# Optimization experiments

Hardware: AMD Instinct MI355X
Metric: run time of the kernel (lower is better)

The kernel has to match this reference:

```python
import jax, jax.numpy as jnp
import numpy as np

B, H, L, N = 8, 512, 2048, 64  # batch, channels (vmapped width), seq len (l_max), state size
DT_MIN, DT_MAX = 0.01, 1.0


def setup_inputs() -> dict:
    key = jax.random.key(0)
    k1, k2, k3 = jax.random.split(key, 3)
    u = jax.random.normal(k1, (B, H, L), dtype=jnp.float32)
    # 'lin' scaling init: A_re = -0.5, A_im = pi * arange(N), per channel
    A_re = -0.5 * jnp.ones((H, N), jnp.float32)
    A_im = jnp.pi * jnp.broadcast_to(jnp.arange(N, dtype=jnp.float32), (H, N))
    C = jax.random.normal(k2, (H, N, 2), jnp.float32) * jnp.float32(0.5 ** 0.5)
    D = jnp.ones((H,), jnp.float32)
    log_step = (jax.random.uniform(k3, (H,), jnp.float32)
                * (jnp.log(DT_MAX) - jnp.log(DT_MIN)) + jnp.log(DT_MIN))
    return dict(u=u, A_re=A_re, A_im=A_im, C=C, D=D, log_step=log_step)


def reference(u, A_re, A_im, C, D, log_step):
    Lq = u.shape[-1]
    # A = clip(A_re, max=-1e-4) + i*A_im  (H, N) complex
    A = jnp.minimum(A_re, -1e-4) + 1j * A_im
    Cc = C[..., 0] + 1j * C[..., 1]                 # (H, N)
    step = jnp.exp(log_step)                        # (H,)
    dtA = step[:, None] * A                         # (H, N)
    # ZOH kernel: K[h,l] = Re( sum_n C[h,n] * (exp(dtA)-1)/A * exp(dtA)^l )
    coef = Cc * (jnp.exp(dtA) - 1.0) / A            # (H, N)
    ells = jnp.arange(Lq, dtype=jnp.float32)
    expmat = jnp.exp(dtA[:, :, None] * ells)        # (H, N, L) complex
    K = jnp.einsum('hn,hnl->hl', coef, expmat).real  # (H, L)
    # FFT causal convolution: pad to 2L (as in the original: pad u by len(K), K by len(u))
    n2 = 2 * Lq
    Ud = jnp.fft.rfft(u, n=n2, axis=-1)             # (B, H, L+1)
    Kd = jnp.fft.rfft(K, n=n2, axis=-1)             # (H, L+1)
    conv = jnp.fft.irfft(Ud * Kd[None], n=n2, axis=-1)[..., :Lq]
    return conv + D[None, :, None] * u
```

## Files before the change

### kernel.cpp

```cpp
#include <hip/hip_runtime.h>
#include <math.h>


typedef short bf16x8 __attribute__((ext_vector_type(8)));
typedef float f32x4  __attribute__((ext_vector_type(4)));

#define NCHK 32
#define USTR 68
#define ESTR 72

__device__ __forceinline__ short f2bf(float x){
    unsigned u = __float_as_uint(x);
    u += 0x7FFFu + ((u >> 16) & 1u);
    return (short)(u >> 16);
}
__device__ __forceinline__ float bf2f(short h){
    return __uint_as_float(((unsigned)(unsigned short)h) << 16);
}

__global__ void __launch_bounds__(256) s4d_mfma(
    const float* __restrict__ u_g, const float* __restrict__ A_re,
    const float* __restrict__ A_im, const float* __restrict__ Cg,
    const float* __restrict__ Dp, const float* __restrict__ log_step,
    float* __restrict__ out, int B, int H, int L)
{
    const int h    = blockIdx.x;
    const int tid  = threadIdx.x;
    const int wv   = tid >> 6;
    const int lane = tid & 63;
    const int l15  = lane & 15;
    const int oct  = lane >> 4;

    __shared__ __align__(16) float u_s[2][NCHK][USTR];
    __shared__ __align__(16) float w_s[2][NCHK][USTR];
    __shared__ __align__(16) float S_s[2][NCHK][USTR];
    __shared__ __align__(16) short E_s[2][65][ESTR];
    __shared__ float K_s[64];

    const float dt = expf(log_step[h]);

    const float are = fminf(A_re[h*64 + lane], -1e-4f);
    const float aim = A_im[h*64 + lane];
    const float dre = dt * are, dim = dt * aim;
    float sn_, cs_;
    const float er = expf(dre);
    sincosf(dim, &sn_, &cs_);
    const float rre = er * cs_, rim = er * sn_;
    const float den = are*are + aim*aim;
    const float ir  = are/den, ii = -aim/den;
    const float c0r = Cg[(h*64+lane)*2 + 0];
    const float c0i = Cg[(h*64+lane)*2 + 1];
    const float e1r = rre - 1.0f, e1i = rim;
    const float ttr = e1r*ir - e1i*ii;
    const float tti = e1r*ii + e1i*ir;
    const float cre = c0r*ttr - c0i*tti;
    const float cim = c0r*tti + c0i*ttr;

    {
        const float* up = u_g + (size_t)h * (size_t)L;
        float4 a0 = *(const float4*)(up + tid*8);
        float4 a1 = *(const float4*)(up + tid*8 + 4);
        const int ch = (tid*8) >> 6, t0 = (tid*8) & 63;
        *(float4*)&u_s[0][ch][t0]   = a0;
        *(float4*)&u_s[0][ch][t0+4] = a1;
    }

    {
        float qre = rre, qim = rim;
        #pragma unroll
        for (int i=0;i<4;++i){ float t2 = qre*qre - qim*qim; qim = 2.0f*qre*qim; qre = t2; }
        float wre = 1.0f, wim = 0.0f;
        for (int i=0;i<wv;++i){ float t2 = wre*qre - wim*qim; wim = wre*qim + wim*qre; wre = t2; }
        float mre = cre*wre - cim*wim;
        float mim = cre*wim + cim*wre;
        #pragma unroll
        for (int jj=0;jj<16;++jj){
            const int p = wv*16 + jj;
            float red = mre;
            #pragma unroll
            for (int off=32; off; off>>=1) red += __shfl_xor(red, off);
            if (lane == 0) K_s[p] = red;
            E_s[0][p][lane] = f2bf(mre);
            E_s[1][p][lane] = f2bf(-mim);
            const float t2 = mre*rre - mim*rim;
            mim = mre*rim + mim*rre; mre = t2;
        }
        if (wv == 3){ E_s[0][64][lane] = f2bf(mre); E_s[1][64][lane] = f2bf(-mim); }
    }
    __syncthreads();

    bf16x8 Wre[2], Wim[2], Mre[2], Mni[2], Tf[2];
    {
        const int nw = wv*16 + l15;
        const float aw = fminf(A_re[h*64+nw], -1e-4f);
        const float bw = A_im[h*64+nw];
        const float dr = dt*aw, di = dt*bw;
        float s1, c1;
        const float e1 = expf(dr); sincosf(di, &s1, &c1);
        const float rwr = e1*c1, rwi = e1*s1;
        #pragma unroll
        for (int kh=0; kh<2; ++kh){
            const int elo = 63 - (kh*32 + oct*8) - 7;
            float s2, c2;
            const float e2 = expf(dr*(float)elo); sincosf(di*(float)elo, &s2, &c2);
            float vr = e2*c2, vi = e2*s2;
            Wre[kh][7] = f2bf(vr); Wim[kh][7] = f2bf(vi);
            #pragma unroll
            for (int i=6;i>=0;--i){
                const float t2 = vr*rwr - vi*rwi;
                vi = vr*rwi + vi*rwr; vr = t2;
                Wre[kh][i] = f2bf(vr); Wim[kh][i] = f2bf(vi);
            }
        }
        const int jp1 = wv*16 + l15 + 1;
        #pragma unroll
        for (int kh=0; kh<2; ++kh){
            Mre[kh] = *(const bf16x8*)&E_s[0][jp1][kh*32 + oct*8];
            Mni[kh] = *(const bf16x8*)&E_s[1][jp1][kh*32 + oct*8];
            #pragma unroll
            for (int i=0;i<8;++i){
                const int t = kh*32 + oct*8 + i;
                const int d = (wv*16 + l15) - t;
                Tf[kh][i] = (d >= 0) ? f2bf(K_s[d]) : (short)0;
            }
        }
    }
    float rhor = 0.0f, rhoi = 0.0f;
    if (wv == 0){
        float s3, c3;
        const float e3 = expf(dre * 64.0f); sincosf(dim * 64.0f, &s3, &c3);
        rhor = e3*c3; rhoi = e3*s3;
    }
    const float Dh = Dp[h];

    for (int b=0; b<B; ++b){
        const int buf = b & 1;
        const size_t obase = ((size_t)b*H + h) * (size_t)L;
        float4 p0 = {0,0,0,0}, p1 = {0,0,0,0};
        const bool pf = (b+1 < B);
        if (pf){
            const float* up = u_g + ((size_t)(b+1)*H + h) * (size_t)L;
            p0 = *(const float4*)(up + tid*8);
            p1 = *(const float4*)(up + tid*8 + 4);
        }
        bf16x8 Uh[2][2], Ul[2][2];
        #pragma unroll
        for (int ct=0; ct<2; ++ct){
            const int ch = ct*16 + l15;
            #pragma unroll
            for (int kh=0; kh<2; ++kh){
                const float4 x0 = *(const float4*)&u_s[buf][ch][kh*32 + oct*8];
                const float4 x1 = *(const float4*)&u_s[buf][ch][kh*32 + oct*8 + 4];
                const float f[8] = {x0.x,x0.y,x0.z,x0.w,x1.x,x1.y,x1.z,x1.w};
                #pragma unroll
                for (int i=0;i<8;++i){
                    const short hi = f2bf(f[i]);
                    Uh[ct][kh][i] = hi;
                    Ul[ct][kh][i] = f2bf(f[i] - bf2f(hi));
                }
            }
        }
        #pragma unroll
        for (int ct=0; ct<2; ++ct){
            f32x4 ar = {0.f,0.f,0.f,0.f}, ai2 = {0.f,0.f,0.f,0.f};
            #pragma unroll
            for (int kh=0; kh<2; ++kh){
                ar  = __builtin_amdgcn_mfma_f32_16x16x32_bf16(Wre[kh], Uh[ct][kh], ar, 0,0,0);
                ar  = __builtin_amdgcn_mfma_f32_16x16x32_bf16(Wre[kh], Ul[ct][kh], ar, 0,0,0);
                ai2 = __builtin_amdgcn_mfma_f32_16x16x32_bf16(Wim[kh], Uh[ct][kh], ai2, 0,0,0);
                ai2 = __builtin_amdgcn_mfma_f32_16x16x32_bf16(Wim[kh], Ul[ct][kh], ai2, 0,0,0);
            }
            const int ch = ct*16 + l15;
            const int n0 = wv*16 + oct*4;
            *(float4*)&w_s[0][ch][n0] = *(float4*)&ar;
            *(float4*)&w_s[1][ch][n0] = *(float4*)&ai2;
        }
        __syncthreads();
        if (wv == 0){
            float sr = 0.0f, si = 0.0f;
            #pragma unroll 4
            for (int k=0;k<NCHK;++k){
                S_s[0][k][lane] = sr; S_s[1][k][lane] = si;
                const float wr = w_s[0][k][lane];
                const float wi = w_s[1][k][lane];
                const float t2 = rhor*sr - rhoi*si + wr;
                si = rhor*si + rhoi*sr + wi;
                sr = t2;
            }
        }
        __syncthreads();
        #pragma unroll
        for (int ct=0; ct<2; ++ct){
            const int ch = ct*16 + l15;
            bf16x8 Srh[2], Srl[2], Sih[2], Sil[2];
            #pragma unroll
            for (int kh=0; kh<2; ++kh){
                {
                    const float4 x0 = *(const float4*)&S_s[0][ch][kh*32+oct*8];
                    const float4 x1 = *(const float4*)&S_s[0][ch][kh*32+oct*8+4];
                    const float f[8] = {x0.x,x0.y,x0.z,x0.w,x1.x,x1.y,x1.z,x1.w};
                    #pragma unroll
                    for (int i=0;i<8;++i){
                        const short hi = f2bf(f[i]);
                        Srh[kh][i] = hi;
                        Srl[kh][i] = f2bf(f[i] - bf2f(hi));
                    }
                }
                {
                    const float4 x0 = *(const float4*)&S_s[1][ch][kh*32+oct*8];
                    const float4 x1 = *(const float4*)&S_s[1][ch][kh*32+oct*8+4];
                    const float f[8] = {x0.x,x0.y,x0.z,x0.w,x1.x,x1.y,x1.z,x1.w};
                    #pragma unroll
                    for (int i=0;i<8;++i){
                        const short hi = f2bf(f[i]);
                        Sih[kh][i] = hi;
                        Sil[kh][i] = f2bf(f[i] - bf2f(hi));
                    }
                }
            }
            f32x4 acc = {0.f,0.f,0.f,0.f};
            #pragma unroll
            for (int kh=0; kh<2; ++kh){
                acc = __builtin_amdgcn_mfma_f32_16x16x32_bf16(Mre[kh], Srh[kh], acc, 0,0,0);
                acc = __builtin_amdgcn_mfma_f32_16x16x32_bf16(Mre[kh], Srl[kh], acc, 0,0,0);
                acc = __builtin_amdgcn_mfma_f32_16x16x32_bf16(Mni[kh], Sih[kh], acc, 0,0,0);
                acc = __builtin_amdgcn_mfma_f32_16x16x32_bf16(Mni[kh], Sil[kh], acc, 0,0,0);
                acc = __builtin_amdgcn_mfma_f32_16x16x32_bf16(Tf[kh],  Uh[ct][kh], acc, 0,0,0);
                acc = __builtin_amdgcn_mfma_f32_16x16x32_bf16(Tf[kh],  Ul[ct][kh], acc, 0,0,0);
            }
            const int j0 = wv*16 + oct*4;
            const float4 uu = *(const float4*)&u_s[buf][ch][j0];
            float4 y;
            y.x = acc[0] + Dh*uu.x;
            y.y = acc[1] + Dh*uu.y;
            y.z = acc[2] + Dh*uu.z;
            y.w = acc[3] + Dh*uu.w;
            *(float4*)(out + obase + (size_t)(ch*64 + j0)) = y;
        }
        if (pf){
            const int ch = (tid*8) >> 6, t0 = (tid*8) & 63;
            *(float4*)&u_s[buf^1][ch][t0]   = p0;
            *(float4*)&u_s[buf^1][ch][t0+4] = p1;
        }
        __syncthreads();
    }
}

extern "C" void kernel_launch(void* const* d_in, const int* in_sizes, int n_in,
                              void* d_out, int out_size, void* d_ws, size_t ws_size,
                              hipStream_t stream) {
    const float* u        = (const float*)d_in[0];
    const float* A_re     = (const float*)d_in[1];
    const float* A_im     = (const float*)d_in[2];
    const float* C        = (const float*)d_in[3];
    const float* Dp       = (const float*)d_in[4];
    const float* log_step = (const float*)d_in[5];
    float* out = (float*)d_out;

    const int H = in_sizes[4];
    const int L = 2048;
    const int B = in_sizes[0] / (H * L);
    (void)d_ws; (void)ws_size; (void)out_size; (void)n_in;

    dim3 grid(H);
    dim3 block(256);
    hipLaunchKernelGGL(s4d_mfma, grid, block, 0, stream,
                       u, A_re, A_im, C, Dp, log_step, out, B, H, L);
}
```

Before: 49.76 us.

## Split MFMA operators into hi/lo bf16 pairs and alias shared buffers

The W, M and Toeplitz operator matrices are now split into high and low bf16 parts, with a third MFMA term per product, so both operands keep near-fp32 precision. The E staging buffer is stored as fp32 and shares a pooled LDS region with w_s and S_s, which cuts the block's shared memory. Launch bounds now ask for 3 blocks per CU. rho is computed by repeated squaring, and the diagonal K[0] is folded into the D skip term. The extra MFMAs and the added register pressure from the duplicated operand fragments are the cost paid for the accuracy and the higher occupancy.

```diff
diff --git a/kernel.cpp b/kernel.cpp
--- a/kernel.cpp
+++ b/kernel.cpp
@@ -7,18 +7,32 @@
 
 #define NCHK 32
 #define USTR 68
-#define ESTR 72
-
-__device__ __forceinline__ short f2bf(float x){
+#define ESTR 66
+#define MFMA __builtin_amdgcn_mfma_f32_16x16x32_bf16
+
+static __device__ __forceinline__ short f2bf(float x){
     unsigned u = __float_as_uint(x);
     u += 0x7FFFu + ((u >> 16) & 1u);
     return (short)(u >> 16);
 }
-__device__ __forceinline__ float bf2f(short h){
+static __device__ __forceinline__ float bf2f(short h){
     return __uint_as_float(((unsigned)(unsigned short)h) << 16);
 }
-
-__global__ void __launch_bounds__(256) s4d_mfma(
+static __device__ __forceinline__ void split8(const float* f, bf16x8& hi, bf16x8& lo){
+    #pragma unroll
+    for (int i=0;i<8;++i){
+        const short hv = f2bf(f[i]);
+        hi[i] = hv;
+        lo[i] = f2bf(f[i] - bf2f(hv));
+    }
+}
+static __device__ __forceinline__ void cmul(float& xr, float& xi, float yr, float yi){
+    const float t = xr*yr - xi*yi;
+    xi = xr*yi + xi*yr;
+    xr = t;
+}
+
+__global__ void __launch_bounds__(256, 3) s4d_mfma4(
     const float* __restrict__ u_g, const float* __restrict__ A_re,
     const float* __restrict__ A_im, const float* __restrict__ Cg,
     const float* __restrict__ Dp, const float* __restrict__ log_step,
@@ -32,10 +46,12 @@
     const int oct  = lane >> 4;
 
     __shared__ __align__(16) float u_s[2][NCHK][USTR];
-    __shared__ __align__(16) float w_s[2][NCHK][USTR];
-    __shared__ __align__(16) float S_s[2][NCHK][USTR];
-    __shared__ __align__(16) short E_s[2][65][ESTR];
+    __shared__ __align__(16) char  pool2[34816];
     __shared__ float K_s[64];
+
+    float (*w_s)[NCHK][USTR] = (float (*)[NCHK][USTR])pool2;
+    float (*S_s)[NCHK][USTR] = (float (*)[NCHK][USTR])(pool2 + 17408);
+    float* Ef = (float*)pool2;
 
     const float dt = expf(log_step[h]);
 
@@ -65,12 +81,16 @@
         *(float4*)&u_s[0][ch][t0+4] = a1;
     }
 
+    float rhor, rhoi;
     {
         float qre = rre, qim = rim;
         #pragma unroll
-        for (int i=0;i<4;++i){ float t2 = qre*qre - qim*qim; qim = 2.0f*qre*qim; qre = t2; }
+        for (int i=0;i<4;++i){ const float t2=qre*qre-qim*qim; qim=2.0f*qre*qim; qre=t2; }
+        rhor = qre; rhoi = qim;
+        cmul(rhor, rhoi, rhor, rhoi);
+        cmul(rhor, rhoi, rhor, rhoi);
         float wre = 1.0f, wim = 0.0f;
-        for (int i=0;i<wv;++i){ float t2 = wre*qre - wim*qim; wim = wre*qim + wim*qre; wre = t2; }
+        for (int i=0;i<wv;++i) cmul(wre, wim, qre, qim);
         float mre = cre*wre - cim*wim;
         float mim = cre*wim + cim*wre;
         #pragma unroll
@@ -80,23 +100,26 @@
             #pragma unroll
             for (int off=32; off; off>>=1) red += __shfl_xor(red, off);
             if (lane == 0) K_s[p] = red;
-            E_s[0][p][lane] = f2bf(mre);
-            E_s[1][p][lane] = f2bf(-mim);
-            const float t2 = mre*rre - mim*rim;
-            mim = mre*rim + mim*rre; mre = t2;
-        }
-        if (wv == 3){ E_s[0][64][lane] = f2bf(mre); E_s[1][64][lane] = f2bf(-mim); }
+            Ef[p*ESTR + lane]      = mre;
+            Ef[(65+p)*ESTR + lane] = -mim;
+            cmul(mre, mim, rre, rim);
+        }
+        if (wv == 3){
+            Ef[64*ESTR + lane]      = mre;
+            Ef[(65+64)*ESTR + lane] = -mim;
+        }
     }
     __syncthreads();
 
-    bf16x8 Wre[2], Wim[2], Mre[2], Mni[2], Tf[2];
+    bf16x8 Whre[2], Wlre[2], Whim[2], Wlim[2];
+    bf16x8 Mhre[2], Mlre[2], Mhni[2], Mlni[2];
+    bf16x8 Th[2],  Tl[2];
     {
         const int nw = wv*16 + l15;
         const float aw = fminf(A_re[h*64+nw], -1e-4f);
         const float bw = A_im[h*64+nw];
         const float dr = dt*aw, di = dt*bw;
-        float s1, c1;
-        const float e1 = expf(dr); sincosf(di, &s1, &c1);
+        float s1, c1; const float e1 = expf(dr); sincosf(di, &s1, &c1);
         const float rwr = e1*c1, rwi = e1*s1;
         #pragma unroll
         for (int kh=0; kh<2; ++kh){
@@ -104,34 +127,38 @@
             float s2, c2;
             const float e2 = expf(dr*(float)elo); sincosf(di*(float)elo, &s2, &c2);
             float vr = e2*c2, vi = e2*s2;
-            Wre[kh][7] = f2bf(vr); Wim[kh][7] = f2bf(vi);
+            float fr[8], fi[8];
+            fr[7] = vr; fi[7] = vi;
             #pragma unroll
             for (int i=6;i>=0;--i){
-                const float t2 = vr*rwr - vi*rwi;
-                vi = vr*rwi + vi*rwr; vr = t2;
-                Wre[kh][i] = f2bf(vr); Wim[kh][i] = f2bf(vi);
-            }
+                cmul(vr, vi, rwr, rwi);
+                fr[i] = vr; fi[i] = vi;
+            }
+            split8(fr, Whre[kh], Wlre[kh]);
+            split8(fi, Whim[kh], Wlim[kh]);
         }
         const int jp1 = wv*16 + l15 + 1;
         #pragma unroll
         for (int kh=0; kh<2; ++kh){
-            Mre[kh] = *(const bf16x8*)&E_s[0][jp1][kh*32 + oct*8];
-            Mni[kh] = *(const bf16x8*)&E_s[1][jp1][kh*32 + oct*8];
+            const int n0 = kh*32 + oct*8;
+            float fm[8];
+            #pragma unroll
+            for (int i=0;i<8;++i) fm[i] = Ef[jp1*ESTR + n0 + i];
+            split8(fm, Mhre[kh], Mlre[kh]);
+            #pragma unroll
+            for (int i=0;i<8;++i) fm[i] = Ef[(65+jp1)*ESTR + n0 + i];
+            split8(fm, Mhni[kh], Mlni[kh]);
+            float ft[8];
             #pragma unroll
             for (int i=0;i<8;++i){
-                const int t = kh*32 + oct*8 + i;
-                const int d = (wv*16 + l15) - t;
-                Tf[kh][i] = (d >= 0) ? f2bf(K_s[d]) : (short)0;
-            }
-        }
-    }
-    float rhor = 0.0f, rhoi = 0.0f;
-    if (wv == 0){
-        float s3, c3;
-        const float e3 = expf(dre * 64.0f); sincosf(dim * 64.0f, &s3, &c3);
-        rhor = e3*c3; rhoi = e3*s3;
-    }
-    const float Dh = Dp[h];
+                const int d = (wv*16 + l15) - (n0 + i);
+                ft[i] = (d > 0) ? K_s[d] : 0.0f;
+            }
+            split8(ft, Th[kh], Tl[kh]);
+        }
+    }
+    const float DK = Dp[h] + K_s[0];
+    __syncthreads();
 
     for (int b=0; b<B; ++b){
         const int buf = b & 1;
@@ -152,28 +179,25 @@
                 const float4 x0 = *(const float4*)&u_s[buf][ch][kh*32 + oct*8];
                 const float4 x1 = *(const float4*)&u_s[buf][ch][kh*32 + oct*8 + 4];
                 const float f[8] = {x0.x,x0.y,x0.z,x0.w,x1.x,x1.y,x1.z,x1.w};
-                #pragma unroll
-                for (int i=0;i<8;++i){
-                    const short hi = f2bf(f[i]);
-                    Uh[ct][kh][i] = hi;
-                    Ul[ct][kh][i] = f2bf(f[i] - bf2f(hi));
-                }
+                split8(f, Uh[ct][kh], Ul[ct][kh]);
             }
         }
         #pragma unroll
         for (int ct=0; ct<2; ++ct){
-            f32x4 ar = {0.f,0.f,0.f,0.f}, ai2 = {0.f,0.f,0.f,0.f};
-            #pragma unroll
-            for (int kh=0; kh<2; ++kh){
-                ar  = __builtin_amdgcn_mfma_f32_16x16x32_bf16(Wre[kh], Uh[ct][kh], ar, 0,0,0);
-                ar  = __builtin_amdgcn_mfma_f32_16x16x32_bf16(Wre[kh], Ul[ct][kh], ar, 0,0,0);
-                ai2 = __builtin_amdgcn_mfma_f32_16x16x32_bf16(Wim[kh], Uh[ct][kh], ai2, 0,0,0);
-                ai2 = __builtin_amdgcn_mfma_f32_16x16x32_bf16(Wim[kh], Ul[ct][kh], ai2, 0,0,0);
+            f32x4 ar = {0.f,0.f,0.f,0.f}, ai = {0.f,0.f,0.f,0.f};
+            #pragma unroll
+            for (int kh=0; kh<2; ++kh){
+                ar = MFMA(Whre[kh], Uh[ct][kh], ar, 0,0,0);
+                ar = MFMA(Whre[kh], Ul[ct][kh], ar, 0,0,0);
+                ar = MFMA(Wlre[kh], Uh[ct][kh], ar, 0,0,0);
+                ai = MFMA(Whim[kh], Uh[ct][kh], ai, 0,0,0);
+                ai = MFMA(Whim[kh], Ul[ct][kh], ai, 0,0,0);
+                ai = MFMA(Wlim[kh], Uh[ct][kh], ai, 0,0,0);
             }
             const int ch = ct*16 + l15;
             const int n0 = wv*16 + oct*4;
-            *(float4*)&w_s[0][ch][n0] = *(float4*)&ar;
-            *(float4*)&w_s[1][ch][n0] = *(float4*)&ai2;
+            *(f32x4*)&w_s[0][ch][n0] = ar;
+            *(f32x4*)&w_s[1][ch][n0] = ai;
         }
         __syncthreads();
         if (wv == 0){
@@ -183,8 +207,8 @@
                 S_s[0][k][lane] = sr; S_s[1][k][lane] = si;
                 const float wr = w_s[0][k][lane];
                 const float wi = w_s[1][k][lane];
-                const float t2 = rhor*sr - rhoi*si + wr;
-                si = rhor*si + rhoi*sr + wi;
+                const float t2 = fmaf(rhor, sr, fmaf(-rhoi, si, wr));
+                si = fmaf(rhor, si, fmaf(rhoi, sr, wi));
                 sr = t2;
             }
         }
@@ -199,48 +223,41 @@
                     const float4 x0 = *(const float4*)&S_s[0][ch][kh*32+oct*8];
                     const float4 x1 = *(const float4*)&S_s[0][ch][kh*32+oct*8+4];
                     const float f[8] = {x0.x,x0.y,x0.z,x0.w,x1.x,x1.y,x1.z,x1.w};
-                    #pragma unroll
-                    for (int i=0;i<8;++i){
-                        const short hi = f2bf(f[i]);
-                        Srh[kh][i] = hi;
-                        Srl[kh][i] = f2bf(f[i] - bf2f(hi));
-                    }
+                    split8(f, Srh[kh], Srl[kh]);
                 }
                 {
                     const float4 x0 = *(const float4*)&S_s[1][ch][kh*32+oct*8];
                     const float4 x1 = *(const float4*)&S_s[1][ch][kh*32+oct*8+4];
                     const float f[8] = {x0.x,x0.y,x0.z,x0.w,x1.x,x1.y,x1.z,x1.w};
-                    #pragma unroll
-                    for (int i=0;i<8;++i){
-                        const short hi = f2bf(f[i]);
-                        Sih[kh][i] = hi;
-                        Sil[kh][i] = f2bf(f[i] - bf2f(hi));
-                    }
+                    split8(f, Sih[kh], Sil[kh]);
                 }
             }
             f32x4 acc = {0.f,0.f,0.f,0.f};
             #pragma unroll
             for (int kh=0; kh<2; ++kh){
-                acc = __builtin_amdgcn_mfma_f32_16x16x32_bf16(Mre[kh], Srh[kh], acc, 0,0,0);
-                acc = __builtin_amdgcn_mfma_f32_16x16x32_bf16(Mre[kh], Srl[kh], acc, 0,0,0);
-                acc = __builtin_amdgcn_mfma_f32_16x16x32_bf16(Mni[kh], Sih[kh], acc, 0,0,0);
-                acc = __builtin_amdgcn_mfma_f32_16x16x32_bf16(Mni[kh], Sil[kh], acc, 0,0,0);
-                acc = __builtin_amdgcn_mfma_f32_16x16x32_bf16(Tf[kh],  Uh[ct][kh], acc, 0,0,0);
-                acc = __builtin_amdgcn_mfma_f32_16x16x32_bf16(Tf[kh],  Ul[ct][kh], acc, 0,0,0);
+                acc = MFMA(Mhre[kh], Srh[kh], acc, 0,0,0);
+                acc = MFMA(Mhre[kh], Srl[kh], acc, 0,0,0);
+                acc = MFMA(Mlre[kh], Srh[kh], acc, 0,0,0);
+                acc = MFMA(Mhni[kh], Sih[kh], acc, 0,0,0);
+                acc = MFMA(Mhni[kh], Sil[kh], acc, 0,0,0);
+                acc = MFMA(Mlni[kh], Sih[kh], acc, 0,0,0);
+                acc = MFMA(Th[kh], Uh[ct][kh], acc, 0,0,0);
+                acc = MFMA(Th[kh], Ul[ct][kh], acc, 0,0,0);
+                acc = MFMA(Tl[kh], Uh[ct][kh], acc, 0,0,0);
             }
             const int j0 = wv*16 + oct*4;
             const float4 uu = *(const float4*)&u_s[buf][ch][j0];
             float4 y;
-            y.x = acc[0] + Dh*uu.x;
-            y.y = acc[1] + Dh*uu.y;
-            y.z = acc[2] + Dh*uu.z;
-            y.w = acc[3] + Dh*uu.w;
+            y.x = acc[0] + DK*uu.x;
+            y.y = acc[1] + DK*uu.y;
+            y.z = acc[2] + DK*uu.z;
+            y.w = acc[3] + DK*uu.w;
             *(float4*)(out + obase + (size_t)(ch*64 + j0)) = y;
         }
         if (pf){
-            const int ch = (tid*8) >> 6, t0 = (tid*8) & 63;
-            *(float4*)&u_s[buf^1][ch][t0]   = p0;
-            *(float4*)&u_s[buf^1][ch][t0+4] = p1;
+            const int ch2 = (tid*8) >> 6, t0 = (tid*8) & 63;
+            *(float4*)&u_s[buf^1][ch2][t0]   = p0;
+            *(float4*)&u_s[buf^1][ch2][t0+4] = p1;
         }
         __syncthreads();
     }
@@ -264,6 +281,6 @@
 
     dim3 grid(H);
     dim3 block(256);
-    hipLaunchKernelGGL(s4d_mfma, grid, block, 0, stream,
+    hipLaunchKernelGGL(s4d_mfma4, grid, block, 0, stream,
                        u, A_re, A_im, C, Dp, log_step, out, B, H, L);
 }
```

Result: slower. 56.46 us (+13.5%).
